# Performance work log

Measured on AMD Instinct MI355X. Metric: run time of the kernel, lower is better.

The kernel has to match this reference:

```python
import jax, jax.numpy as jnp
import numpy as np

DIM = 1024
N_HEADS = 16
D_K = DIM // N_HEADS
B, N = 2, 2048


def _pairwise_dist(p):
    # p: [B, N, 3] -> Euclidean cdist [B, N, N], grad-safe at zero distance
    sq = jnp.sum(p * p, axis=-1)                      # [B, N]
    d2 = sq[:, :, None] + sq[:, None, :] - 2.0 * jnp.einsum('bnd,bmd->bnm', p, p)
    d2 = jnp.maximum(d2, 0.0)
    safe = jnp.where(d2 > 0.0, d2, 1.0)
    return jnp.where(d2 > 0.0, jnp.sqrt(safe), 0.0)


def setup_inputs() -> dict:
    key = jax.random.key(0)
    ks = jax.random.split(key, 11)
    s = 1.0 / np.sqrt(DIM)
    inp = {
        'x': jax.random.normal(ks[0], (B, N, DIM), jnp.float32),
        'positions': jax.random.normal(ks[1], (B, N, 3), jnp.float32),
        'W_q': jax.random.normal(ks[2], (DIM, DIM), jnp.float32) * s,
        'b_q': jnp.zeros((DIM,), jnp.float32),
        'W_k': jax.random.normal(ks[3], (DIM, DIM), jnp.float32) * s,
        'b_k': jnp.zeros((DIM,), jnp.float32),
        'W_v': jax.random.normal(ks[4], (DIM, DIM), jnp.float32) * s,
        'b_v': jnp.zeros((DIM,), jnp.float32),
        'W_o': jax.random.normal(ks[5], (DIM, DIM), jnp.float32) * s,
        'b_o': jnp.zeros((DIM,), jnp.float32),
        'dist_bias': jax.random.normal(ks[6], (N_HEADS, 1, 1), jnp.float32),
    }
    return inp


def reference(x, positions, W_q, b_q, W_k, b_k, W_v, b_v, W_o, b_o, dist_bias):
    Bv, Nv, C = x.shape
    def proj(W, b):
        # [B,N,C] -> [B,H,N,d_k]
        return (x @ W.T + b).reshape(Bv, Nv, N_HEADS, D_K).transpose(0, 2, 1, 3)
    Q = proj(W_q, b_q)
    K = proj(W_k, b_k)
    V = proj(W_v, b_v)
    attn = jnp.einsum('bhnd,bhmd->bhnm', Q, K) / np.sqrt(D_K)  # [B,H,N,N]
    dists = _pairwise_dist(positions)                          # [B,N,N]
    # log(exp(-|b|*d) + 1e-8), per-head bias broadcast over [B,H,N,N]
    dist_weights = jnp.exp(-jnp.abs(dist_bias)[None] * dists[:, None])
    attn = attn + jnp.log(dist_weights + 1e-8)
    attn = jax.nn.softmax(attn, axis=-1)
    out = jnp.einsum('bhnm,bhmd->bhnd', attn, V)               # [B,H,N,d_k]
    out = out.transpose(0, 2, 1, 3).reshape(Bv, Nv, C)
    return out @ W_o.T + b_o
```

## Files before the change

### kernel.cpp

```cpp
#include <hip/hip_runtime.h>
#include <hip/hip_bf16.h>
#include <stdint.h>

using bf16   = __hip_bfloat16;
using short8 = __attribute__((ext_vector_type(8))) short;
using f32x4  = __attribute__((ext_vector_type(4))) float;
using f32x16 = __attribute__((ext_vector_type(16))) float;

#define NSEQ   2048
#define NHEADS 16
#define DK     64
#define DMODEL 1024
#define LOG2E  1.44269504088896f

#define GLDS16(gp, lp) __builtin_amdgcn_global_load_lds( \
    (const __attribute__((address_space(1))) void*)(gp), \
    (__attribute__((address_space(3))) void*)(lp), 16, 0, 0)

__device__ __forceinline__ ushort f2bf(float f){
  bf16 h = __float2bfloat16(f);
  return __builtin_bit_cast(ushort, h);
}
__device__ __forceinline__ float bf2f(ushort u){
  uint t = ((uint)u)<<16; return __builtin_bit_cast(float, t);
}

__global__ void k_cvt_all(const float4* __restrict__ x,  const float4* __restrict__ wq,
                          const float4* __restrict__ wk, const float4* __restrict__ wv,
                          const float4* __restrict__ wo,
                          ushort4* __restrict__ xb,  ushort4* __restrict__ wqb,
                          ushort4* __restrict__ wkb, ushort4* __restrict__ wvb,
                          ushort4* __restrict__ wob){
  const int i = blockIdx.x*blockDim.x + threadIdx.x;
  const float4* s; ushort4* d; int off;
  if (i < 1048576){ s = x; d = xb; off = i; }
  else {
    const int wi = i - 1048576;
    const int w  = wi >> 18;
    off = wi & 262143;
    switch(w){
      case 0:  s = wq; d = wqb; break;
      case 1:  s = wk; d = wkb; break;
      case 2:  s = wv; d = wvb; break;
      default: s = wo; d = wob; break;
    }
  }
  float4 v = s[off];
  ushort4 o;
  o.x = f2bf(v.x); o.y = f2bf(v.y); o.z = f2bf(v.z); o.w = f2bf(v.w);
  d[off] = o;
}

__global__ void k_geo(const float* __restrict__ pos, ushort* __restrict__ AF,
                      ushort* __restrict__ BF, int n){
  int i = blockIdx.x*blockDim.x + threadIdx.x;
  if (i >= n) return;
  float x = pos[i*3+0], y = pos[i*3+1], z = pos[i*3+2];
  float sq = x*x + y*y + z*z;
  ushort xh = f2bf(x);  float xhf = bf2f(xh);  ushort xl = f2bf(x - xhf);
  ushort yh = f2bf(y);  float yhf = bf2f(yh);  ushort yl = f2bf(y - yhf);
  ushort zh = f2bf(z);  float zhf = bf2f(zh);  ushort zl = f2bf(z - zhf);
  ushort sh = f2bf(sq); float shf = bf2f(sh);  ushort sl = f2bf(sq - shf);
  ushort m2xh = f2bf(-2.f*xhf), m2xl = f2bf(-2.f*bf2f(xl));
  ushort m2yh = f2bf(-2.f*yhf), m2yl = f2bf(-2.f*bf2f(yl));
  ushort m2zh = f2bf(-2.f*zhf), m2zl = f2bf(-2.f*bf2f(zl));
  const ushort one = 0x3F80;
  ushort af[16] = {xh,xl,xh, yh,yl,yh, zh,zl,zh, sh,sl, one,one, 0,0,0};
  ushort bv[16] = {m2xh,m2xh,m2xl, m2yh,m2yh,m2yl, m2zh,m2zh,m2zl, one,one, sh,sl, 0,0,0};
  *(uint4*)&AF[i*16]     = *(uint4*)&af[0];
  *(uint4*)&AF[i*16 + 8] = *(uint4*)&af[8];
  *(uint4*)&BF[i*16]     = *(uint4*)&bv[0];
  *(uint4*)&BF[i*16 + 8] = *(uint4*)&bv[8];
}

__device__ __forceinline__ void gemm_core(
    const ushort* __restrict__ Ap, const ushort* __restrict__ Bp,
    int bm, int bn, int tid, ushort smem[2][2][4096], f32x4 (&acc)[4][4])
{
  const int wave = tid>>6, lane = tid&63;
  const int wr = wave>>1, wc = wave&1;
  const int ko   = (lane>>4)*8;
  const int srow = wave*16 + (lane>>2);
  const int scol = (lane&3)*8;

  const ushort* As = Ap + (size_t)(bm*128)*DMODEL + scol;
  const ushort* Bs = Bp + (size_t)(bn*128)*DMODEL + scol;

#define STAGEG(buf, kt) do { \
    _Pragma("unroll") \
    for (int i_=0;i_<2;i_++){ \
      GLDS16(As + (size_t)(i_*64 + srow)*DMODEL + (kt)*32, &smem[buf][0][i_*2048 + wave*512]); \
      GLDS16(Bs + (size_t)(i_*64 + srow)*DMODEL + (kt)*32, &smem[buf][1][i_*2048 + wave*512]); \
    } } while(0)

  STAGEG(0, 0);
  for (int kt=0; kt<32; ++kt){
    int cur = kt&1;
    __syncthreads();
    if (kt<31) STAGEG(cur^1, kt+1);
    short8 af[4], bfv[4];
    const ushort* At = smem[cur][0];
    const ushort* Bt = smem[cur][1];
    #pragma unroll
    for (int mi=0;mi<4;mi++) af[mi]  = *(const short8*)&At[(wr*64+mi*16+(lane&15))*32 + ko];
    #pragma unroll
    for (int ni=0;ni<4;ni++) bfv[ni] = *(const short8*)&Bt[(wc*64+ni*16+(lane&15))*32 + ko];
    #pragma unroll
    for (int mi=0;mi<4;mi++)
      #pragma unroll
      for (int ni=0;ni<4;ni++)
        acc[mi][ni] = __builtin_amdgcn_mfma_f32_16x16x32_bf16(af[mi], bfv[ni], acc[mi][ni], 0,0,0);
  }
#undef STAGEG
}

__global__ __launch_bounds__(256) void k_gemm_qkv(
    const ushort* __restrict__ xb,
    const ushort* __restrict__ Wqb, const ushort* __restrict__ Wkb, const ushort* __restrict__ Wvb,
    const float* __restrict__ bq, const float* __restrict__ bk, const float* __restrict__ bv,
    ushort* __restrict__ Qo, ushort* __restrict__ Ko, ushort* __restrict__ Vto)
{
  __shared__ ushort smem[2][2][4096];
  const int tid = threadIdx.x;
  const int work = (blockIdx.x & 7)*96 + (blockIdx.x >> 3);
  const int t = work & 255;
  const int z = work >> 8;
  const int lane = tid&63, wave = tid>>6;
  const int wr = wave>>1, wc = wave&1;

  const ushort* Ap; const ushort* Bp; const float* bias;
  ushort* outp; int bm, bn; float scale = 1.0f;
  if (z==0){ Ap=xb;  Bp=Wqb; bias=bq; outp=Qo;  bm=t>>3; bn=t&7; scale=0.125f*LOG2E; }
  else if (z==1){ Ap=xb;  Bp=Wkb; bias=bk; outp=Ko;  bm=t>>3; bn=t&7; }
  else          { Ap=Wvb; Bp=xb;  bias=bv; outp=Vto; bm=t&7;  bn=t>>3; }

  f32x4 acc[4][4] = {};
  gemm_core(Ap, Bp, bm, bn, tid, smem, acc);

  if (z<2){
    #pragma unroll
    for (int mi=0;mi<4;mi++){
      const int m0 = bm*128 + wr*64 + mi*16 + (lane>>4)*4;
      #pragma unroll
      for (int ni=0;ni<4;ni++){
        const int nn = bn*128 + wc*64 + ni*16 + (lane&15);
        const float bs = bias[nn];
        const int h = nn>>6, d = nn&63;
        #pragma unroll
        for (int j=0;j<4;j++){
          int mm = m0+j;
          int b = mm>>11, nr = mm&2047;
          size_t off = (((size_t)(b*NHEADS+h)*NSEQ) + nr)*DK + d;
          outp[off] = f2bf((acc[mi][ni][j] + bs)*scale);
        }
      }
    }
  } else {
    #pragma unroll
    for (int mi=0;mi<4;mi++){
      const int m0 = bm*128 + wr*64 + mi*16 + (lane>>4)*4;
      #pragma unroll
      for (int ni=0;ni<4;ni++){
        const int nn = bn*128 + wc*64 + ni*16 + (lane&15);
        const int b = nn>>11, nr = nn&2047;
        #pragma unroll
        for (int j=0;j<4;j++){
          int mm = m0+j;
          const float bs = bias[mm];
          int h = mm>>6, d = mm&63;
          size_t off = (((size_t)(b*NHEADS+h)*DK) + d)*NSEQ + nr;
          outp[off] = f2bf(acc[mi][ni][j] + bs);
        }
      }
    }
  }
}

__global__ __launch_bounds__(256) void k_gemm_out(
    const ushort* __restrict__ Ob, const ushort* __restrict__ Wob,
    const float* __restrict__ bo, float* __restrict__ out)
{
  __shared__ ushort smem[2][2][4096];
  const int tid = threadIdx.x;
  const int work = (blockIdx.x & 7)*32 + (blockIdx.x >> 3);
  const int lane = tid&63, wave = tid>>6;
  const int wr = wave>>1, wc = wave&1;
  const int bm = work>>3, bn = work&7;
  f32x4 acc[4][4] = {};
  gemm_core(Ob, Wob, bm, bn, tid, smem, acc);
  #pragma unroll
  for (int mi=0;mi<4;mi++){
    const int m0 = bm*128 + wr*64 + mi*16 + (lane>>4)*4;
    #pragma unroll
    for (int ni=0;ni<4;ni++){
      const int nn = bn*128 + wc*64 + ni*16 + (lane&15);
      const float bs = bo[nn];
      #pragma unroll
      for (int j=0;j<4;j++)
        out[(size_t)(m0+j)*DMODEL + nn] = acc[mi][ni][j] + bs;
    }
  }
}

__global__ __launch_bounds__(256) void k_attn(
    const ushort* __restrict__ Q, const ushort* __restrict__ K, const ushort* __restrict__ Vt,
    const ushort* __restrict__ AF, const ushort* __restrict__ BF,
    const float* __restrict__ dist_bias,
    ushort* __restrict__ O)
{
  __shared__ ushort kb[2][4096];
  __shared__ ushort vb[2][4096];
  const int tid = threadIdx.x, wave = tid>>6, lane = tid&63;
  const int work = ((blockIdx.x & 7) << 6) | (blockIdx.x >> 3);
  const int qt = work & 15, h = (work >> 4) & 15, b = work >> 8;
  const int lo5 = lane&31, hi = lane>>5;
  const float ah2 = fabsf(dist_bias[h]) * LOG2E;
  const ushort* Qh  = Q  + ((size_t)(b*NHEADS+h))*NSEQ*DK;
  const ushort* Kh  = K  + ((size_t)(b*NHEADS+h))*NSEQ*DK;
  const ushort* Vth = Vt + ((size_t)(b*NHEADS+h))*DK*NSEQ;
  const ushort* AFb = AF + (size_t)b*NSEQ*16;
  const ushort* BFb = BF + (size_t)b*NSEQ*16;

  const int q0 = qt*128 + wave*32;

  short8 qf[4];
  #pragma unroll
  for (int s=0;s<4;s++)
    qf[s] = *(const short8*)&Qh[(size_t)(q0+lo5)*DK + s*16 + hi*8];
  const short8 bfq = *(const short8*)&BFb[(size_t)(q0+lo5)*16 + hi*8];

  const int grow  = lane>>3;
  const int gc16  = (lane&7) ^ grow;
  const int rowb  = wave*8 + grow;

#define STAGE(buf, jb) do { \
    _Pragma("unroll") \
    for (int p_=0;p_<2;p_++){ \
      const int rw_ = p_*32 + rowb; \
      GLDS16(Kh  + (size_t)((jb)+rw_)*DK   + gc16*8, &kb[buf][(p_*256 + wave*64)*8]); \
      GLDS16(Vth + (size_t)rw_*NSEQ + (jb) + gc16*8, &vb[buf][(p_*256 + wave*64)*8]); \
    } } while(0)

  const int rb = lo5*64;
  const int rx = lo5 & 7;

  f32x16 o0 = {}, o1 = {};
  float l_run = 0.f;

  STAGE(0, 0);
  for (int t=0; t<32; ++t){
    const int cur = t&1;
    __syncthreads();
    if (t<31) STAGE(cur^1, (t+1)*64);
    const ushort* kbc = kb[cur];
    const ushort* vbc = vb[cur];
    #pragma unroll
    for (int ss=0; ss<2; ++ss){
      const int jb = t*64 + ss*32;
      const short8 afk = *(const short8*)&AFb[(size_t)(jb+lo5)*16 + hi*8];
      f32x16 zz = {};
      f32x16 d2 = __builtin_amdgcn_mfma_f32_32x32x16_bf16(afk, bfq, zz, 0,0,0);
      const short8 kf0 = *(const short8*)&kbc[ss*2048 + rb + (((0+hi)^rx)<<3)];
      const short8 kf1 = *(const short8*)&kbc[ss*2048 + rb + (((2+hi)^rx)<<3)];
      const short8 kf2 = *(const short8*)&kbc[ss*2048 + rb + (((4+hi)^rx)<<3)];
      const short8 kf3 = *(const short8*)&kbc[ss*2048 + rb + (((6+hi)^rx)<<3)];
      f32x16 st = {};
      st = __builtin_amdgcn_mfma_f32_32x32x16_bf16(kf0, qf[0], st, 0,0,0);
      st = __builtin_amdgcn_mfma_f32_32x32x16_bf16(kf1, qf[1], st, 0,0,0);
      st = __builtin_amdgcn_mfma_f32_32x32x16_bf16(kf2, qf[2], st, 0,0,0);
      st = __builtin_amdgcn_mfma_f32_32x32x16_bf16(kf3, qf[3], st, 0,0,0);
      float p[16];
      #pragma unroll
      for (int r=0;r<16;r++){
        float d = __builtin_amdgcn_sqrtf(fmaxf(d2[r], 0.f));
        p[r] = __builtin_exp2f(fmaf(-ah2, d, st[r]));
      }
      float s01=p[0]+p[1], s23=p[2]+p[3], s45=p[4]+p[5], s67=p[6]+p[7];
      float s89=p[8]+p[9], sab=p[10]+p[11], scd=p[12]+p[13], sef=p[14]+p[15];
      float rsum = ((s01+s23)+(s45+s67)) + ((s89+sab)+(scd+sef));
      rsum += __shfl_xor(rsum, 32);
      l_run += rsum;
      #pragma unroll
      for (int s=0;s<2;s++){
        uint w0, w1, w2, w3;
        asm("v_cvt_pk_bf16_f32 %0, %1, %2" : "=v"(w0) : "v"(p[8*s+0]), "v"(p[8*s+1]));
        asm("v_cvt_pk_bf16_f32 %0, %1, %2" : "=v"(w2) : "v"(p[8*s+4]), "v"(p[8*s+5]));
        asm("v_cvt_pk_bf16_f32 %0, %1, %2" : "=v"(w1) : "v"(p[8*s+2]), "v"(p[8*s+3]));
        asm("v_cvt_pk_bf16_f32 %0, %1, %2" : "=v"(w3) : "v"(p[8*s+6]), "v"(p[8*s+7]));
        asm volatile("v_permlane32_swap_b32 %0, %1" : "+v"(w0), "+v"(w2));
        asm volatile("v_permlane32_swap_b32 %0, %1" : "+v"(w1), "+v"(w3));
        uint4 aw; aw.x = w0; aw.y = w1; aw.z = w2; aw.w = w3;
        const short8 pa = __builtin_bit_cast(short8, aw);
        const int jcol = (ss<<2) + 2*s + hi;
        const short8 v0 = *(const short8*)&vbc[       rb + ((jcol^rx)<<3)];
        const short8 v1 = *(const short8*)&vbc[2048 + rb + ((jcol^rx)<<3)];
        o0 = __builtin_amdgcn_mfma_f32_32x32x16_bf16(pa, v0, o0, 0,0,0);
        o1 = __builtin_amdgcn_mfma_f32_32x32x16_bf16(pa, v1, o1, 0,0,0);
      }
    }
  }
#undef STAGE

  #pragma unroll
  for (int r=0;r<16;r++){
    const int src = (r&3) + 8*(r>>2) + 4*hi;
    const float lr = __shfl(l_run, src);
    const float inv = 1.f/lr;
    const int i = q0 + src;
    O[((size_t)b*NSEQ + i)*DMODEL + h*DK + lo5]      = f2bf(o0[r]*inv);
    O[((size_t)b*NSEQ + i)*DMODEL + h*DK + 32 + lo5] = f2bf(o1[r]*inv);
  }
}

extern "C" void kernel_launch(void* const* d_in, const int* in_sizes, int n_in,
                              void* d_out, int out_size, void* d_ws, size_t ws_size,
                              hipStream_t stream) {
  const float* x   = (const float*)d_in[0];
  const float* pos = (const float*)d_in[1];
  const float* Wq  = (const float*)d_in[2];
  const float* bq  = (const float*)d_in[3];
  const float* Wk  = (const float*)d_in[4];
  const float* bk  = (const float*)d_in[5];
  const float* Wv  = (const float*)d_in[6];
  const float* bv  = (const float*)d_in[7];
  const float* Wo  = (const float*)d_in[8];
  const float* bo  = (const float*)d_in[9];
  const float* db  = (const float*)d_in[10];
  float* out = (float*)d_out;

  char* ws = (char*)d_ws;
  ushort* xb   = (ushort*)(ws);
  ushort* Wqb  = (ushort*)(ws + ((size_t)8<<20));
  ushort* Wkb  = (ushort*)(ws + ((size_t)10<<20));
  ushort* Wvb  = (ushort*)(ws + ((size_t)12<<20));
  ushort* Wob  = (ushort*)(ws + ((size_t)14<<20));
  ushort* Qb   = (ushort*)(ws + ((size_t)16<<20));
  ushort* Kb   = (ushort*)(ws + ((size_t)24<<20));
  ushort* Vtb  = (ushort*)(ws + ((size_t)32<<20));
  ushort* AFt  = Wqb;
  ushort* BFt  = (ushort*)(ws + ((size_t)8<<20) + (128<<10));
  ushort* Omrg = xb;

  k_cvt_all<<<10240, 256, 0, stream>>>(
      (const float4*)x, (const float4*)Wq, (const float4*)Wk, (const float4*)Wv, (const float4*)Wo,
      (ushort4*)xb, (ushort4*)Wqb, (ushort4*)Wkb, (ushort4*)Wvb, (ushort4*)Wob);
  k_gemm_qkv<<<768, 256, 0, stream>>>(xb, Wqb, Wkb, Wvb, bq, bk, bv, Qb, Kb, Vtb);
  k_geo<<<16, 256, 0, stream>>>(pos, AFt, BFt, 2*NSEQ);
  k_attn<<<512, 256, 0, stream>>>(Qb, Kb, Vtb, AFt, BFt, db, Omrg);
  k_gemm_out<<<256, 256, 0, stream>>>(Omrg, Wob, bo, out);
}
```

Baseline: 243.5 us.

## Fuse geometry prep into convert kernel, retile output GEMM, stage AF in LDS

Folds the positional-feature kernel into the conversion kernel as extra blocks and moves its output to a dedicated workspace region, removing one launch. The output projection moves from 128x128 to 128x64 tiles (512 blocks) with its own inlined loop, so more blocks are available to fill the CUs. The attention kernel stages the per-key distance features through LDS alongside K/V instead of reading them from global memory. It also raises wave priority around the MFMA sections and drops the XCD-aware block swizzle in favour of a 3D grid. The smaller output tiles reload the A operand more often, and the lost swizzle may hurt L2 locality.

```diff
diff --git a/kernel.cpp b/kernel.cpp
--- a/kernel.cpp
+++ b/kernel.cpp
@@ -25,12 +25,35 @@
   uint t = ((uint)u)<<16; return __builtin_bit_cast(float, t);
 }
 
-__global__ void k_cvt_all(const float4* __restrict__ x,  const float4* __restrict__ wq,
+__global__ void k_cvt_geo(const float4* __restrict__ x,  const float4* __restrict__ wq,
                           const float4* __restrict__ wk, const float4* __restrict__ wv,
                           const float4* __restrict__ wo,
                           ushort4* __restrict__ xb,  ushort4* __restrict__ wqb,
                           ushort4* __restrict__ wkb, ushort4* __restrict__ wvb,
-                          ushort4* __restrict__ wob){
+                          ushort4* __restrict__ wob,
+                          const float* __restrict__ pos,
+                          ushort* __restrict__ AF, ushort* __restrict__ BF){
+  if (blockIdx.x >= 10240){
+    const int i = (blockIdx.x - 10240)*blockDim.x + threadIdx.x;
+    if (i >= 2*NSEQ) return;
+    float px = pos[i*3+0], py = pos[i*3+1], pz = pos[i*3+2];
+    float sq = px*px + py*py + pz*pz;
+    ushort xh = f2bf(px); float xhf = bf2f(xh); ushort xl = f2bf(px - xhf);
+    ushort yh = f2bf(py); float yhf = bf2f(yh); ushort yl = f2bf(py - yhf);
+    ushort zh = f2bf(pz); float zhf = bf2f(zh); ushort zl = f2bf(pz - zhf);
+    ushort sh = f2bf(sq); float shf = bf2f(sh); ushort sl = f2bf(sq - shf);
+    ushort m2xh = f2bf(-2.f*xhf), m2xl = f2bf(-2.f*bf2f(xl));
+    ushort m2yh = f2bf(-2.f*yhf), m2yl = f2bf(-2.f*bf2f(yl));
+    ushort m2zh = f2bf(-2.f*zhf), m2zl = f2bf(-2.f*bf2f(zl));
+    const ushort one = 0x3F80;
+    ushort af[16] = {xh,xl,xh, yh,yl,yh, zh,zl,zh, sh,sl, one,one, 0,0,0};
+    ushort bv[16] = {m2xh,m2xh,m2xl, m2yh,m2yh,m2yl, m2zh,m2zh,m2zl, one,one, sh,sl, 0,0,0};
+    *(uint4*)&AF[i*16]     = *(uint4*)&af[0];
+    *(uint4*)&AF[i*16 + 8] = *(uint4*)&af[8];
+    *(uint4*)&BF[i*16]     = *(uint4*)&bv[0];
+    *(uint4*)&BF[i*16 + 8] = *(uint4*)&bv[8];
+    return;
+  }
   const int i = blockIdx.x*blockDim.x + threadIdx.x;
   const float4* s; ushort4* d; int off;
   if (i < 1048576){ s = x; d = xb; off = i; }
@@ -49,28 +72,6 @@
   ushort4 o;
   o.x = f2bf(v.x); o.y = f2bf(v.y); o.z = f2bf(v.z); o.w = f2bf(v.w);
   d[off] = o;
-}
-
-__global__ void k_geo(const float* __restrict__ pos, ushort* __restrict__ AF,
-                      ushort* __restrict__ BF, int n){
-  int i = blockIdx.x*blockDim.x + threadIdx.x;
-  if (i >= n) return;
-  float x = pos[i*3+0], y = pos[i*3+1], z = pos[i*3+2];
-  float sq = x*x + y*y + z*z;
-  ushort xh = f2bf(x);  float xhf = bf2f(xh);  ushort xl = f2bf(x - xhf);
-  ushort yh = f2bf(y);  float yhf = bf2f(yh);  ushort yl = f2bf(y - yhf);
-  ushort zh = f2bf(z);  float zhf = bf2f(zh);  ushort zl = f2bf(z - zhf);
-  ushort sh = f2bf(sq); float shf = bf2f(sh);  ushort sl = f2bf(sq - shf);
-  ushort m2xh = f2bf(-2.f*xhf), m2xl = f2bf(-2.f*bf2f(xl));
-  ushort m2yh = f2bf(-2.f*yhf), m2yl = f2bf(-2.f*bf2f(yl));
-  ushort m2zh = f2bf(-2.f*zhf), m2zl = f2bf(-2.f*bf2f(zl));
-  const ushort one = 0x3F80;
-  ushort af[16] = {xh,xl,xh, yh,yl,yh, zh,zl,zh, sh,sl, one,one, 0,0,0};
-  ushort bv[16] = {m2xh,m2xh,m2xl, m2yh,m2yh,m2yl, m2zh,m2zh,m2zl, one,one, sh,sl, 0,0,0};
-  *(uint4*)&AF[i*16]     = *(uint4*)&af[0];
-  *(uint4*)&AF[i*16 + 8] = *(uint4*)&af[8];
-  *(uint4*)&BF[i*16]     = *(uint4*)&bv[0];
-  *(uint4*)&BF[i*16 + 8] = *(uint4*)&bv[8];
 }
 
 __device__ __forceinline__ void gemm_core(
@@ -180,20 +181,51 @@
     const ushort* __restrict__ Ob, const ushort* __restrict__ Wob,
     const float* __restrict__ bo, float* __restrict__ out)
 {
-  __shared__ ushort smem[2][2][4096];
+  __shared__ ushort sa[2][4096];
+  __shared__ ushort sb[2][2048];
   const int tid = threadIdx.x;
-  const int work = (blockIdx.x & 7)*32 + (blockIdx.x >> 3);
+  const int work = (blockIdx.x & 7)*64 + (blockIdx.x >> 3);
+  const int bm = work>>4, bn = work&15;
   const int lane = tid&63, wave = tid>>6;
   const int wr = wave>>1, wc = wave&1;
-  const int bm = work>>3, bn = work&7;
-  f32x4 acc[4][4] = {};
-  gemm_core(Ob, Wob, bm, bn, tid, smem, acc);
+  const int ko   = (lane>>4)*8;
+  const int srow = wave*16 + (lane>>2);
+  const int scol = (lane&3)*8;
+
+  const ushort* As = Ob  + (size_t)(bm*128)*DMODEL + scol;
+  const ushort* Bs = Wob + (size_t)(bn*64)*DMODEL + scol;
+
+#define STAGEO(buf, kt) do { \
+    _Pragma("unroll") \
+    for (int i_=0;i_<2;i_++) \
+      GLDS16(As + (size_t)(i_*64 + srow)*DMODEL + (kt)*32, &sa[buf][i_*2048 + wave*512]); \
+    GLDS16(Bs + (size_t)srow*DMODEL + (kt)*32, &sb[buf][wave*512]); \
+  } while(0)
+
+  f32x4 acc[4][2] = {};
+  STAGEO(0, 0);
+  for (int kt=0; kt<32; ++kt){
+    int cur = kt&1;
+    __syncthreads();
+    if (kt<31) STAGEO(cur^1, kt+1);
+    short8 af[4], bfv[2];
+    #pragma unroll
+    for (int mi=0;mi<4;mi++) af[mi]  = *(const short8*)&sa[cur][(wr*64+mi*16+(lane&15))*32 + ko];
+    #pragma unroll
+    for (int ni=0;ni<2;ni++) bfv[ni] = *(const short8*)&sb[cur][(wc*32+ni*16+(lane&15))*32 + ko];
+    #pragma unroll
+    for (int mi=0;mi<4;mi++)
+      #pragma unroll
+      for (int ni=0;ni<2;ni++)
+        acc[mi][ni] = __builtin_amdgcn_mfma_f32_16x16x32_bf16(af[mi], bfv[ni], acc[mi][ni], 0,0,0);
+  }
+#undef STAGEO
   #pragma unroll
   for (int mi=0;mi<4;mi++){
     const int m0 = bm*128 + wr*64 + mi*16 + (lane>>4)*4;
     #pragma unroll
-    for (int ni=0;ni<4;ni++){
-      const int nn = bn*128 + wc*64 + ni*16 + (lane&15);
+    for (int ni=0;ni<2;ni++){
+      const int nn = bn*64 + wc*32 + ni*16 + (lane&15);
       const float bs = bo[nn];
       #pragma unroll
       for (int j=0;j<4;j++)
@@ -210,9 +242,9 @@
 {
   __shared__ ushort kb[2][4096];
   __shared__ ushort vb[2][4096];
+  __shared__ ushort ab[2][1024];
   const int tid = threadIdx.x, wave = tid>>6, lane = tid&63;
-  const int work = ((blockIdx.x & 7) << 6) | (blockIdx.x >> 3);
-  const int qt = work & 15, h = (work >> 4) & 15, b = work >> 8;
+  const int qt = blockIdx.x, h = blockIdx.y, b = blockIdx.z;
   const int lo5 = lane&31, hi = lane>>5;
   const float ah2 = fabsf(dist_bias[h]) * LOG2E;
   const ushort* Qh  = Q  + ((size_t)(b*NHEADS+h))*NSEQ*DK;
@@ -239,7 +271,10 @@
       const int rw_ = p_*32 + rowb; \
       GLDS16(Kh  + (size_t)((jb)+rw_)*DK   + gc16*8, &kb[buf][(p_*256 + wave*64)*8]); \
       GLDS16(Vth + (size_t)rw_*NSEQ + (jb) + gc16*8, &vb[buf][(p_*256 + wave*64)*8]); \
-    } } while(0)
+    } \
+    if (wave < 2) \
+      GLDS16(AFb + (size_t)((jb) + wave*32 + (lane>>1))*16 + (lane&1)*8, &ab[buf][wave*512]); \
+  } while(0)
 
   const int rb = lo5*64;
   const int rx = lo5 & 7;
@@ -254,21 +289,23 @@
     if (t<31) STAGE(cur^1, (t+1)*64);
     const ushort* kbc = kb[cur];
     const ushort* vbc = vb[cur];
+    const ushort* abc = ab[cur];
     #pragma unroll
     for (int ss=0; ss<2; ++ss){
-      const int jb = t*64 + ss*32;
-      const short8 afk = *(const short8*)&AFb[(size_t)(jb+lo5)*16 + hi*8];
+      const short8 afk = *(const short8*)&abc[(ss*32+lo5)*16 + hi*8];
       f32x16 zz = {};
       f32x16 d2 = __builtin_amdgcn_mfma_f32_32x32x16_bf16(afk, bfq, zz, 0,0,0);
       const short8 kf0 = *(const short8*)&kbc[ss*2048 + rb + (((0+hi)^rx)<<3)];
       const short8 kf1 = *(const short8*)&kbc[ss*2048 + rb + (((2+hi)^rx)<<3)];
       const short8 kf2 = *(const short8*)&kbc[ss*2048 + rb + (((4+hi)^rx)<<3)];
       const short8 kf3 = *(const short8*)&kbc[ss*2048 + rb + (((6+hi)^rx)<<3)];
+      __builtin_amdgcn_s_setprio(1);
       f32x16 st = {};
       st = __builtin_amdgcn_mfma_f32_32x32x16_bf16(kf0, qf[0], st, 0,0,0);
       st = __builtin_amdgcn_mfma_f32_32x32x16_bf16(kf1, qf[1], st, 0,0,0);
       st = __builtin_amdgcn_mfma_f32_32x32x16_bf16(kf2, qf[2], st, 0,0,0);
       st = __builtin_amdgcn_mfma_f32_32x32x16_bf16(kf3, qf[3], st, 0,0,0);
+      __builtin_amdgcn_s_setprio(0);
       float p[16];
       #pragma unroll
       for (int r=0;r<16;r++){
@@ -280,6 +317,7 @@
       float rsum = ((s01+s23)+(s45+s67)) + ((s89+sab)+(scd+sef));
       rsum += __shfl_xor(rsum, 32);
       l_run += rsum;
+      __builtin_amdgcn_s_setprio(1);
       #pragma unroll
       for (int s=0;s<2;s++){
         uint w0, w1, w2, w3;
@@ -297,6 +335,7 @@
         o0 = __builtin_amdgcn_mfma_f32_32x32x16_bf16(pa, v0, o0, 0,0,0);
         o1 = __builtin_amdgcn_mfma_f32_32x32x16_bf16(pa, v1, o1, 0,0,0);
       }
+      __builtin_amdgcn_s_setprio(0);
     }
   }
 #undef STAGE
@@ -337,15 +376,15 @@
   ushort* Qb   = (ushort*)(ws + ((size_t)16<<20));
   ushort* Kb   = (ushort*)(ws + ((size_t)24<<20));
   ushort* Vtb  = (ushort*)(ws + ((size_t)32<<20));
-  ushort* AFt  = Wqb;
-  ushort* BFt  = (ushort*)(ws + ((size_t)8<<20) + (128<<10));
+  ushort* AFt  = (ushort*)(ws + ((size_t)40<<20));
+  ushort* BFt  = (ushort*)(ws + ((size_t)40<<20) + (128<<10));
   ushort* Omrg = xb;
 
-  k_cvt_all<<<10240, 256, 0, stream>>>(
+  k_cvt_geo<<<10256, 256, 0, stream>>>(
       (const float4*)x, (const float4*)Wq, (const float4*)Wk, (const float4*)Wv, (const float4*)Wo,
-      (ushort4*)xb, (ushort4*)Wqb, (ushort4*)Wkb, (ushort4*)Wvb, (ushort4*)Wob);
+      (ushort4*)xb, (ushort4*)Wqb, (ushort4*)Wkb, (ushort4*)Wvb, (ushort4*)Wob,
+      pos, AFt, BFt);
   k_gemm_qkv<<<768, 256, 0, stream>>>(xb, Wqb, Wkb, Wvb, bq, bk, bv, Qb, Kb, Vtb);
-  k_geo<<<16, 256, 0, stream>>>(pos, AFt, BFt, 2*NSEQ);
-  k_attn<<<512, 256, 0, stream>>>(Qb, Kb, Vtb, AFt, BFt, db, Omrg);
-  k_gemm_out<<<256, 256, 0, stream>>>(Omrg, Wob, bo, out);
-}
+  k_attn<<<dim3(16,NHEADS,2), 256, 0, stream>>>(Qb, Kb, Vtb, AFt, BFt, db, Omrg);
+  k_gemm_out<<<512, 256, 0, stream>>>(Omrg, Wob, bo, out);
+}
```

After: 247.1 us. No clear change (+1.5%).
